# Performance work log

Measured on AMD Instinct MI355X. Metric: run time of the kernel, lower is better.

Reference implementation:

```python
import jax, jax.numpy as jnp
import numpy as np
from jax import lax

DK, K = 3, 3          # duration_kernel_size, kernel_size
PD, P = 1, 1          # duration_padding, padding
RANKS = 3


def setup_inputs() -> dict:
    key = jax.random.key(0)
    k1, k2, k3, k4, k5 = jax.random.split(key, 5)
    B, Cin, Cout, D, H, W = 2, 64, 64, 8, 128, 128
    x = jax.random.normal(k1, (B, Cin, D, H, W), dtype=jnp.float32)
    # 1x1x1 conv weights (squeezed to [out, in])
    head_w = jax.random.normal(k2, (Cout, Cin), dtype=jnp.float32) * 0.1
    tail_w = jax.random.normal(k3, (Cout, Cout), dtype=jnp.float32) * 0.1
    std = float(np.sqrt(2.0 / RANKS))
    U_w = jax.random.normal(k4, (DK * K * K, RANKS), dtype=jnp.float32) * std
    V_w = jax.random.normal(k5, (Cout, RANKS), dtype=jnp.float32) * std
    return {"x": x, "head_w": head_w, "tail_w": tail_w, "U_w": U_w, "V_w": V_w}


def _forward(x, head_w, tail_w, U_w, V_w):
    B, Cin, D, H, W = x.shape
    Cout = head_w.shape[0]
    R = U_w.shape[1]
    # head 1x1x1 conv
    h = jnp.einsum('bidhw,oi->bodhw', x, head_w)
    # replicate pad (torch F.pad mode='replicate' == jnp.pad mode='edge')
    hp = jnp.pad(h, ((0, 0), (0, 0), (PD, PD), (P, P), (P, P)), mode='edge')
    # einsum('bcdhwk,kr->bcdhwr') over unfolded windows == depthwise conv with
    # a kernel shared across channels: fold (B,C) into the batch dim and run a
    # 1->R channel 3D correlation (avoids materializing the [.,27] unfold tensor).
    xin = hp.reshape(B * Cout, 1, D + 2 * PD, H + 2 * P, W + 2 * P)
    kern = U_w.T.reshape(R, 1, DK, K, K)  # unfold flattens as (dk, kh, kw)
    Up = lax.conv_general_dilated(
        xin, kern, window_strides=(1, 1, 1), padding='VALID',
        dimension_numbers=('NCDHW', 'OIDHW', 'NCDHW'))
    Up = Up.reshape(B, Cout, R, D, H, W)
    # _l2norm over rank dim: u / (1e-6 + ||u||_2)
    norm = jnp.sqrt(jnp.sum(Up * Up, axis=2, keepdims=True))
    Un = Up / (1e-6 + norm)
    # V projection: einsum('bcdhwk,cr->brdhwk') with k==1
    Vp = jnp.einsum('bcdhw,cr->brdhw', h, V_w)
    # UV: einsum('bcdhwr,brdhwk->bcdhwk') with k==1 -> contract over r
    UV = jnp.einsum('bcrdhw,brdhw->bcdhw', Un, Vp)
    # tail 1x1x1 conv
    out = jnp.einsum('bcdhw,oc->bodhw', UV, tail_w)
    return out


def reference(x, head_w, tail_w, U_w, V_w):
    return _forward(x, head_w, tail_w, U_w, V_w)
```

## Files before the change

### kernel.cpp

```cpp
#include <hip/hip_runtime.h>

#define Bn   2
#define Cn   64
#define Dd   8
#define Hd   128
#define Wd   128
#define HW   16384
#define DHW  131072
#define NPOS 262144
#define NELEM 16777216

typedef __attribute__((ext_vector_type(8))) short short8;
typedef __attribute__((ext_vector_type(4))) float floatx4;

__device__ __forceinline__ short f2bf(float f) {
    union { float f; unsigned u; } v; v.f = f;
    unsigned r = (v.u + 0x7FFFu + ((v.u >> 16) & 1u)) >> 16;
    return (short)r;
}
__device__ __forceinline__ float bf2f(short s) {
    union { unsigned u; float f; } v; v.u = ((unsigned)(unsigned short)s) << 16;
    return v.f;
}

__global__ __launch_bounds__(256) void k_prep(const float* __restrict__ head_w,
                                              const float* __restrict__ tail_w,
                                              const float* __restrict__ V_w,
                                              short* __restrict__ Whh, short* __restrict__ Whl,
                                              short* __restrict__ Wth, short* __restrict__ Wtl)
{
    int t = threadIdx.x;
#pragma unroll
    for (int rep = 0; rep < 16; ++rep) {
        int idx = rep * 256 + t;
        float wh = head_w[idx];
        short hh = f2bf(wh);
        Whh[idx] = hh; Whl[idx] = f2bf(wh - bf2f(hh));
        float wt = tail_w[idx];
        short th = f2bf(wt);
        Wth[idx] = th; Wtl[idx] = f2bf(wt - bf2f(th));
    }
    if (t < 192) {
        int r = t >> 6, i = t & 63;
        float s = 0.f;
        for (int cc = 0; cc < 64; ++cc) s += V_w[cc * 3 + r] * head_w[cc * 64 + i];
        short hh = f2bf(s);
        Whh[(64 + r) * 64 + i] = hh;
        Whl[(64 + r) * 64 + i] = f2bf(s - bf2f(hh));
    }
#pragma unroll
    for (int rep = 0; rep < 4; ++rep) {
        int idx = rep * 256 + t;
        if (idx < 832) { Whh[67 * 64 + idx] = 0; Whl[67 * 64 + idx] = 0; }
    }
}

__global__ __launch_bounds__(256) void k_headm(const float* __restrict__ x,
                                               const short* __restrict__ Whh,
                                               const short* __restrict__ Whl,
                                               float* __restrict__ h,
                                               float* __restrict__ Vp)
{
    __shared__ short Xh[16 * 64 * 8], Xl[16 * 64 * 8];
    __shared__ short Bh[10 * 64 * 8], Bl[10 * 64 * 8];
    int t  = threadIdx.x;
    int p0 = blockIdx.x * 128;
    int b  = p0 >> 17;
    int s0 = p0 & (DHW - 1);
    const float* xb = x + ((size_t)b * Cn) * DHW + s0;

    int pp = t & 127;
    int ho = t >> 7;
#pragma unroll
    for (int pass = 0; pass < 4; ++pass) {
        int in0 = pass * 16 + ho * 8;
        short8 vh, vl;
#pragma unroll
        for (int j = 0; j < 8; ++j) {
            float f = xb[(size_t)(in0 + j) * DHW + pp];
            short hh = f2bf(f);
            vh[j] = hh; vl[j] = f2bf(f - bf2f(hh));
        }
        int blk  = ((in0 >> 5) << 3) | (pp >> 4);
        int slot = (((in0 >> 3) & 3) << 4) | (pp & 15);
        *(short8*)&Xh[(blk * 64 + slot) * 8] = vh;
        *(short8*)&Xl[(blk * 64 + slot) * 8] = vl;
    }
#pragma unroll
    for (int pass = 0; pass < 3; ++pass) {
        int unit = pass * 256 + t;
        if (unit < 640) {
            int o   = unit - (unit / 80) * 80;
            int oc  = unit / 80;
            int in0 = oc * 8;
            int blk  = ((o >> 4) << 1) | (in0 >> 5);
            int slot = (((in0 >> 3) & 3) << 4) | (o & 15);
            *(short8*)&Bh[(blk * 64 + slot) * 8] = *(const short8*)&Whh[o * 64 + in0];
            *(short8*)&Bl[(blk * 64 + slot) * 8] = *(const short8*)&Whl[o * 64 + in0];
        }
    }
    __syncthreads();

    int lane = t & 63;
    int w    = t >> 6;
    floatx4 acc[2][5];
#pragma unroll
    for (int mt = 0; mt < 2; ++mt)
#pragma unroll
        for (int nt = 0; nt < 5; ++nt) acc[mt][nt] = (floatx4)0.f;

    const short8* XhV = (const short8*)Xh;
    const short8* XlV = (const short8*)Xl;
    const short8* BhV = (const short8*)Bh;
    const short8* BlV = (const short8*)Bl;
#pragma unroll
    for (int ks = 0; ks < 2; ++ks) {
        short8 ah0 = XhV[(ks * 8 + w * 2 + 0) * 64 + lane];
        short8 ah1 = XhV[(ks * 8 + w * 2 + 1) * 64 + lane];
        short8 al0 = XlV[(ks * 8 + w * 2 + 0) * 64 + lane];
        short8 al1 = XlV[(ks * 8 + w * 2 + 1) * 64 + lane];
#pragma unroll
        for (int nt = 0; nt < 5; ++nt) {
            short8 bh = BhV[(nt * 2 + ks) * 64 + lane];
            short8 bl = BlV[(nt * 2 + ks) * 64 + lane];
            acc[0][nt] = __builtin_amdgcn_mfma_f32_16x16x32_bf16(al0, bl, acc[0][nt], 0, 0, 0);
            acc[0][nt] = __builtin_amdgcn_mfma_f32_16x16x32_bf16(al0, bh, acc[0][nt], 0, 0, 0);
            acc[0][nt] = __builtin_amdgcn_mfma_f32_16x16x32_bf16(ah0, bl, acc[0][nt], 0, 0, 0);
            acc[0][nt] = __builtin_amdgcn_mfma_f32_16x16x32_bf16(ah0, bh, acc[0][nt], 0, 0, 0);
            acc[1][nt] = __builtin_amdgcn_mfma_f32_16x16x32_bf16(al1, bl, acc[1][nt], 0, 0, 0);
            acc[1][nt] = __builtin_amdgcn_mfma_f32_16x16x32_bf16(al1, bh, acc[1][nt], 0, 0, 0);
            acc[1][nt] = __builtin_amdgcn_mfma_f32_16x16x32_bf16(ah1, bl, acc[1][nt], 0, 0, 0);
            acc[1][nt] = __builtin_amdgcn_mfma_f32_16x16x32_bf16(ah1, bh, acc[1][nt], 0, 0, 0);
        }
    }

    int outc = lane & 15;
    int quad = lane >> 4;
#pragma unroll
    for (int mt = 0; mt < 2; ++mt) {
#pragma unroll
        for (int nt = 0; nt < 5; ++nt) {
            int o   = nt * 16 + outc;
            int pos = w * 32 + mt * 16 + quad * 4;
            if (o < 64) {
                *(floatx4*)&h[((size_t)(b * Cn + o)) * DHW + s0 + pos] = acc[mt][nt];
            } else if (o < 67) {
                *(floatx4*)&Vp[((size_t)(b * 3 + (o - 64))) * DHW + s0 + pos] = acc[mt][nt];
            }
        }
    }
}

__global__ __launch_bounds__(256) void k_uv(const float* __restrict__ h,
                                            const float* __restrict__ Vp,
                                            const float* __restrict__ U_w,
                                            float* __restrict__ UV)
{
    __shared__ float tile[Dd][4][Wd];

    int blk = blockIdx.x;
    int yt  = blk & 63;
    int bc  = blk >> 6;
    int b   = bc >> 6;
    int y0  = yt * 2;
    int t   = threadIdx.x;

    const float* hb = h + (size_t)bc * DHW;
#pragma unroll
    for (int rep = 0; rep < 4; ++rep) {
        int idx = rep * 256 + t;
        int d   = idx >> 7;
        int rem = idx & 127;
        int yr  = rem >> 5;
        int x4  = (rem & 31) * 4;
        int zy  = y0 - 1 + yr;
        zy = zy < 0 ? 0 : (zy > Hd - 1 ? Hd - 1 : zy);
        *(floatx4*)&tile[d][yr][x4] = *(const floatx4*)(hb + d * HW + zy * Wd + x4);
    }
    __syncthreads();

    int xx = t & 127;
    int yr = t >> 7;
    int y  = y0 + yr;
    int xm = xx - 1; if (xm < 0) xm = 0;
    int xp = xx + 1; if (xp > Wd - 1) xp = Wd - 1;

    const float* vpb = Vp + (size_t)b * 3 * DHW + y * Wd + xx;
    float* uvb       = UV + (size_t)bc * DHW + y * Wd + xx;

    for (int d = 0; d < Dd; ++d) {
        float up0 = 0.f, up1 = 0.f, up2 = 0.f;
#pragma unroll
        for (int dk = 0; dk < 3; ++dk) {
            int zd = d + dk - 1; zd = zd < 0 ? 0 : (zd > Dd - 1 ? Dd - 1 : zd);
#pragma unroll
            for (int kh = 0; kh < 3; ++kh) {
                const float* row = &tile[zd][yr + kh][0];
                float v0 = row[xm], v1 = row[xx], v2 = row[xp];
                int k0 = (dk * 3 + kh) * 3;
                up0 += v0 * U_w[(k0+0)*3 + 0] + v1 * U_w[(k0+1)*3 + 0] + v2 * U_w[(k0+2)*3 + 0];
                up1 += v0 * U_w[(k0+0)*3 + 1] + v1 * U_w[(k0+1)*3 + 1] + v2 * U_w[(k0+2)*3 + 1];
                up2 += v0 * U_w[(k0+0)*3 + 2] + v1 * U_w[(k0+1)*3 + 2] + v2 * U_w[(k0+2)*3 + 2];
            }
        }
        float nrm = sqrtf(up0 * up0 + up1 * up1 + up2 * up2);
        float inv = 1.f / (1e-6f + nrm);
        float uv = (up0 * vpb[(size_t)d * HW]
                  + up1 * vpb[(size_t)DHW + d * HW]
                  + up2 * vpb[(size_t)2 * DHW + d * HW]) * inv;
        uvb[(size_t)d * HW] = uv;
    }
}

__global__ __launch_bounds__(256) void k_tailm(const float* __restrict__ UV,
                                               const short* __restrict__ Wth,
                                               const short* __restrict__ Wtl,
                                               float* __restrict__ out)
{
    __shared__ short Xh[16 * 64 * 8], Xl[16 * 64 * 8];
    __shared__ short Bh[8 * 64 * 8], Bl[8 * 64 * 8];
    int t  = threadIdx.x;
    int p0 = blockIdx.x * 128;
    int b  = p0 >> 17;
    int s0 = p0 & (DHW - 1);
    const float* ub = UV + ((size_t)b * Cn) * DHW + s0;

    int pp = t & 127;
    int ho = t >> 7;
#pragma unroll
    for (int pass = 0; pass < 4; ++pass) {
        int in0 = pass * 16 + ho * 8;
        short8 vh, vl;
#pragma unroll
        for (int j = 0; j < 8; ++j) {
            float f = ub[(size_t)(in0 + j) * DHW + pp];
            short hh = f2bf(f);
            vh[j] = hh; vl[j] = f2bf(f - bf2f(hh));
        }
        int blk  = ((in0 >> 5) << 3) | (pp >> 4);
        int slot = (((in0 >> 3) & 3) << 4) | (pp & 15);
        *(short8*)&Xh[(blk * 64 + slot) * 8] = vh;
        *(short8*)&Xl[(blk * 64 + slot) * 8] = vl;
    }
#pragma unroll
    for (int pass = 0; pass < 2; ++pass) {
        int unit = pass * 256 + t;
        int o    = unit & 63;
        int oc   = unit >> 6;
        int in0  = oc * 8;
        int blk  = ((o >> 4) << 1) | (in0 >> 5);
        int slot = (((in0 >> 3) & 3) << 4) | (o & 15);
        *(short8*)&Bh[(blk * 64 + slot) * 8] = *(const short8*)&Wth[o * 64 + in0];
        *(short8*)&Bl[(blk * 64 + slot) * 8] = *(const short8*)&Wtl[o * 64 + in0];
    }
    __syncthreads();

    int lane = t & 63;
    int w    = t >> 6;
    floatx4 acc[2][4];
#pragma unroll
    for (int mt = 0; mt < 2; ++mt)
#pragma unroll
        for (int nt = 0; nt < 4; ++nt) acc[mt][nt] = (floatx4)0.f;

    const short8* XhV = (const short8*)Xh;
    const short8* XlV = (const short8*)Xl;
    const short8* BhV = (const short8*)Bh;
    const short8* BlV = (const short8*)Bl;
#pragma unroll
    for (int ks = 0; ks < 2; ++ks) {
        short8 ah0 = XhV[(ks * 8 + w * 2 + 0) * 64 + lane];
        short8 ah1 = XhV[(ks * 8 + w * 2 + 1) * 64 + lane];
        short8 al0 = XlV[(ks * 8 + w * 2 + 0) * 64 + lane];
        short8 al1 = XlV[(ks * 8 + w * 2 + 1) * 64 + lane];
#pragma unroll
        for (int nt = 0; nt < 4; ++nt) {
            short8 bh = BhV[(nt * 2 + ks) * 64 + lane];
            short8 bl = BlV[(nt * 2 + ks) * 64 + lane];
            acc[0][nt] = __builtin_amdgcn_mfma_f32_16x16x32_bf16(al0, bl, acc[0][nt], 0, 0, 0);
            acc[0][nt] = __builtin_amdgcn_mfma_f32_16x16x32_bf16(al0, bh, acc[0][nt], 0, 0, 0);
            acc[0][nt] = __builtin_amdgcn_mfma_f32_16x16x32_bf16(ah0, bl, acc[0][nt], 0, 0, 0);
            acc[0][nt] = __builtin_amdgcn_mfma_f32_16x16x32_bf16(ah0, bh, acc[0][nt], 0, 0, 0);
            acc[1][nt] = __builtin_amdgcn_mfma_f32_16x16x32_bf16(al1, bl, acc[1][nt], 0, 0, 0);
            acc[1][nt] = __builtin_amdgcn_mfma_f32_16x16x32_bf16(al1, bh, acc[1][nt], 0, 0, 0);
            acc[1][nt] = __builtin_amdgcn_mfma_f32_16x16x32_bf16(ah1, bl, acc[1][nt], 0, 0, 0);
            acc[1][nt] = __builtin_amdgcn_mfma_f32_16x16x32_bf16(ah1, bh, acc[1][nt], 0, 0, 0);
        }
    }

    int outc = lane & 15;
    int quad = lane >> 4;
#pragma unroll
    for (int mt = 0; mt < 2; ++mt) {
#pragma unroll
        for (int nt = 0; nt < 4; ++nt) {
            int o   = nt * 16 + outc;
            int pos = w * 32 + mt * 16 + quad * 4;
            *(floatx4*)&out[((size_t)(b * Cn + o)) * DHW + s0 + pos] = acc[mt][nt];
        }
    }
}

extern "C" void kernel_launch(void* const* d_in, const int* in_sizes, int n_in,
                              void* d_out, int out_size, void* d_ws, size_t ws_size,
                              hipStream_t stream)
{
    const float* x      = (const float*)d_in[0];
    const float* head_w = (const float*)d_in[1];
    const float* tail_w = (const float*)d_in[2];
    const float* U_w    = (const float*)d_in[3];
    const float* V_w    = (const float*)d_in[4];
    float* out = (float*)d_out;

    float* h   = (float*)d_ws;
    float* Vp  = h + (size_t)NELEM;
    float* UVf = Vp + (size_t)Bn * 3 * DHW;
    short* Whh = (short*)(UVf + (size_t)NELEM);
    short* Whl = Whh + 80 * 64;
    short* Wth = Whl + 80 * 64;
    short* Wtl = Wth + 64 * 64;

    k_prep<<<1, 256, 0, stream>>>(head_w, tail_w, V_w, Whh, Whl, Wth, Wtl);
    k_headm<<<NPOS / 128, 256, 0, stream>>>(x, Whh, Whl, h, Vp);
    k_uv<<<Bn * Cn * (Hd / 2), 256, 0, stream>>>(h, Vp, U_w, UVf);
    k_tailm<<<NPOS / 128, 256, 0, stream>>>(UVf, Wth, Wtl, out);
}
```

Before: 267.2 us.

## Stage GEMM outputs through LDS for coalesced stores; restructure depth conv reuse

The head and tail MFMA kernels now write accumulators into a padded LDS buffer that aliases the input staging area, then store full 128-position rows per channel with coalesced float4 writes. Before, each lane wrote scattered 16-byte fragments. The depthwise U-conv kernel now loads each depth slice's 3x3 neighbourhood once and scatters its contribution into 8 per-depth accumulators, instead of reloading three slices per output depth. The bf16 hi/lo split switches from round-to-nearest to truncation for the high part, which is cheaper, and the low part still carries the residual. The cost is extra LDS traffic, two more barriers, larger shared memory use and more registers in the conv kernel.

```diff
diff --git a/kernel.cpp b/kernel.cpp
--- a/kernel.cpp
+++ b/kernel.cpp
@@ -22,6 +22,14 @@
     union { unsigned u; float f; } v; v.u = ((unsigned)(unsigned short)s) << 16;
     return v.f;
 }
+__device__ __forceinline__ void split2(float f, short& hi, short& lo) {
+    union { float f; unsigned u; } a; a.f = f;
+    unsigned hu = a.u & 0xFFFF0000u;
+    hi = (short)(hu >> 16);
+    union { unsigned u; float f; } hb; hb.u = hu;
+    union { float f; unsigned u; } lb; lb.f = f - hb.f;
+    lo = (short)(lb.u >> 16);
+}
 
 __global__ __launch_bounds__(256) void k_prep(const float* __restrict__ head_w,
                                               const float* __restrict__ tail_w,
@@ -33,20 +41,20 @@
 #pragma unroll
     for (int rep = 0; rep < 16; ++rep) {
         int idx = rep * 256 + t;
-        float wh = head_w[idx];
-        short hh = f2bf(wh);
-        Whh[idx] = hh; Whl[idx] = f2bf(wh - bf2f(hh));
-        float wt = tail_w[idx];
-        short th = f2bf(wt);
-        Wth[idx] = th; Wtl[idx] = f2bf(wt - bf2f(th));
+        short hh, hl;
+        split2(head_w[idx], hh, hl);
+        Whh[idx] = hh; Whl[idx] = hl;
+        split2(tail_w[idx], hh, hl);
+        Wth[idx] = hh; Wtl[idx] = hl;
     }
     if (t < 192) {
         int r = t >> 6, i = t & 63;
         float s = 0.f;
         for (int cc = 0; cc < 64; ++cc) s += V_w[cc * 3 + r] * head_w[cc * 64 + i];
-        short hh = f2bf(s);
+        short hh, hl;
+        split2(s, hh, hl);
         Whh[(64 + r) * 64 + i] = hh;
-        Whl[(64 + r) * 64 + i] = f2bf(s - bf2f(hh));
+        Whl[(64 + r) * 64 + i] = hl;
     }
 #pragma unroll
     for (int rep = 0; rep < 4; ++rep) {
@@ -61,8 +69,13 @@
                                                float* __restrict__ h,
                                                float* __restrict__ Vp)
 {
-    __shared__ short Xh[16 * 64 * 8], Xl[16 * 64 * 8];
-    __shared__ short Bh[10 * 64 * 8], Bl[10 * 64 * 8];
+    __shared__ __align__(16) char smem[52 * 1024];
+    short* Xh = (short*)smem;
+    short* Xl = (short*)(smem + 16 * 1024);
+    short* Bh = (short*)(smem + 32 * 1024);
+    short* Bl = (short*)(smem + 42 * 1024);
+    float* Cb = (float*)smem;
+
     int t  = threadIdx.x;
     int p0 = blockIdx.x * 128;
     int b  = p0 >> 17;
@@ -77,9 +90,9 @@
         short8 vh, vl;
 #pragma unroll
         for (int j = 0; j < 8; ++j) {
-            float f = xb[(size_t)(in0 + j) * DHW + pp];
-            short hh = f2bf(f);
-            vh[j] = hh; vl[j] = f2bf(f - bf2f(hh));
+            short hh, hl;
+            split2(xb[(size_t)(in0 + j) * DHW + pp], hh, hl);
+            vh[j] = hh; vl[j] = hl;
         }
         int blk  = ((in0 >> 5) << 3) | (pp >> 4);
         int slot = (((in0 >> 3) & 3) << 4) | (pp & 15);
@@ -134,19 +147,29 @@
         }
     }
 
+    __syncthreads();
     int outc = lane & 15;
     int quad = lane >> 4;
 #pragma unroll
-    for (int mt = 0; mt < 2; ++mt) {
+    for (int mt = 0; mt < 2; ++mt)
 #pragma unroll
         for (int nt = 0; nt < 5; ++nt) {
             int o   = nt * 16 + outc;
             int pos = w * 32 + mt * 16 + quad * 4;
-            if (o < 64) {
-                *(floatx4*)&h[((size_t)(b * Cn + o)) * DHW + s0 + pos] = acc[mt][nt];
-            } else if (o < 67) {
-                *(floatx4*)&Vp[((size_t)(b * 3 + (o - 64))) * DHW + s0 + pos] = acc[mt][nt];
-            }
+            *(floatx4*)&Cb[o * 132 + pos] = acc[mt][nt];
+        }
+    __syncthreads();
+
+    int xr = (t & 31) * 4;
+    int ob = t >> 5;
+#pragma unroll
+    for (int pass = 0; pass < 9; ++pass) {
+        int o = pass * 8 + ob;
+        floatx4 vv = *(const floatx4*)&Cb[o * 132 + xr];
+        if (o < 64) {
+            *(floatx4*)&h[((size_t)(b * Cn + o)) * DHW + s0 + xr] = vv;
+        } else if (o < 67) {
+            *(floatx4*)&Vp[((size_t)(b * 3 + (o - 64))) * DHW + s0 + xr] = vv;
         }
     }
 }
@@ -185,29 +208,49 @@
     int xm = xx - 1; if (xm < 0) xm = 0;
     int xp = xx + 1; if (xp > Wd - 1) xp = Wd - 1;
 
+    float a0[8], a1[8], a2[8];
+#pragma unroll
+    for (int d = 0; d < 8; ++d) { a0[d] = 0.f; a1[d] = 0.f; a2[d] = 0.f; }
+
+#define CONTRIB(dd, dk)                                                   \
+    {                                                                     \
+        _Pragma("unroll")                                                 \
+        for (int kh = 0; kh < 3; ++kh) {                                  \
+            _Pragma("unroll")                                             \
+            for (int kw = 0; kw < 3; ++kw) {                              \
+                const int kk = (((dk) * 3 + kh) * 3 + kw) * 3;            \
+                a0[dd] += v[kh][kw] * U_w[kk + 0];                        \
+                a1[dd] += v[kh][kw] * U_w[kk + 1];                        \
+                a2[dd] += v[kh][kw] * U_w[kk + 2];                        \
+            }                                                             \
+        }                                                                 \
+    }
+
+#pragma unroll
+    for (int sl = 0; sl < 8; ++sl) {
+        float v[3][3];
+#pragma unroll
+        for (int kh = 0; kh < 3; ++kh) {
+            const float* row = &tile[sl][yr + kh][0];
+            v[kh][0] = row[xm]; v[kh][1] = row[xx]; v[kh][2] = row[xp];
+        }
+        CONTRIB(sl, 1);
+        if (sl == 0) CONTRIB(0, 0);
+        if (sl < 7)  CONTRIB(sl + 1, 0);
+        if (sl > 0)  CONTRIB(sl - 1, 2);
+        if (sl == 7) CONTRIB(7, 2);
+    }
+#undef CONTRIB
+
     const float* vpb = Vp + (size_t)b * 3 * DHW + y * Wd + xx;
     float* uvb       = UV + (size_t)bc * DHW + y * Wd + xx;
-
-    for (int d = 0; d < Dd; ++d) {
-        float up0 = 0.f, up1 = 0.f, up2 = 0.f;
-#pragma unroll
-        for (int dk = 0; dk < 3; ++dk) {
-            int zd = d + dk - 1; zd = zd < 0 ? 0 : (zd > Dd - 1 ? Dd - 1 : zd);
-#pragma unroll
-            for (int kh = 0; kh < 3; ++kh) {
-                const float* row = &tile[zd][yr + kh][0];
-                float v0 = row[xm], v1 = row[xx], v2 = row[xp];
-                int k0 = (dk * 3 + kh) * 3;
-                up0 += v0 * U_w[(k0+0)*3 + 0] + v1 * U_w[(k0+1)*3 + 0] + v2 * U_w[(k0+2)*3 + 0];
-                up1 += v0 * U_w[(k0+0)*3 + 1] + v1 * U_w[(k0+1)*3 + 1] + v2 * U_w[(k0+2)*3 + 1];
-                up2 += v0 * U_w[(k0+0)*3 + 2] + v1 * U_w[(k0+1)*3 + 2] + v2 * U_w[(k0+2)*3 + 2];
-            }
-        }
-        float nrm = sqrtf(up0 * up0 + up1 * up1 + up2 * up2);
+#pragma unroll
+    for (int d = 0; d < 8; ++d) {
+        float nrm = sqrtf(a0[d] * a0[d] + a1[d] * a1[d] + a2[d] * a2[d]);
         float inv = 1.f / (1e-6f + nrm);
-        float uv = (up0 * vpb[(size_t)d * HW]
-                  + up1 * vpb[(size_t)DHW + d * HW]
-                  + up2 * vpb[(size_t)2 * DHW + d * HW]) * inv;
+        float uv = (a0[d] * vpb[(size_t)d * HW]
+                  + a1[d] * vpb[(size_t)DHW + d * HW]
+                  + a2[d] * vpb[(size_t)2 * DHW + d * HW]) * inv;
         uvb[(size_t)d * HW] = uv;
     }
 }
@@ -217,8 +260,13 @@
                                                const short* __restrict__ Wtl,
                                                float* __restrict__ out)
 {
-    __shared__ short Xh[16 * 64 * 8], Xl[16 * 64 * 8];
-    __shared__ short Bh[8 * 64 * 8], Bl[8 * 64 * 8];
+    __shared__ __align__(16) char smem[48 * 1024];
+    short* Xh = (short*)smem;
+    short* Xl = (short*)(smem + 16 * 1024);
+    short* Bh = (short*)(smem + 32 * 1024);
+    short* Bl = (short*)(smem + 40 * 1024);
+    float* Cb = (float*)smem;
+
     int t  = threadIdx.x;
     int p0 = blockIdx.x * 128;
     int b  = p0 >> 17;
@@ -233,9 +281,9 @@
         short8 vh, vl;
 #pragma unroll
         for (int j = 0; j < 8; ++j) {
-            float f = ub[(size_t)(in0 + j) * DHW + pp];
-            short hh = f2bf(f);
-            vh[j] = hh; vl[j] = f2bf(f - bf2f(hh));
+            short hh, hl;
+            split2(ub[(size_t)(in0 + j) * DHW + pp], hh, hl);
+            vh[j] = hh; vl[j] = hl;
         }
         int blk  = ((in0 >> 5) << 3) | (pp >> 4);
         int slot = (((in0 >> 3) & 3) << 4) | (pp & 15);
@@ -288,16 +336,26 @@
         }
     }
 
+    __syncthreads();
     int outc = lane & 15;
     int quad = lane >> 4;
 #pragma unroll
-    for (int mt = 0; mt < 2; ++mt) {
+    for (int mt = 0; mt < 2; ++mt)
 #pragma unroll
         for (int nt = 0; nt < 4; ++nt) {
             int o   = nt * 16 + outc;
             int pos = w * 32 + mt * 16 + quad * 4;
-            *(floatx4*)&out[((size_t)(b * Cn + o)) * DHW + s0 + pos] = acc[mt][nt];
-        }
+            *(floatx4*)&Cb[o * 132 + pos] = acc[mt][nt];
+        }
+    __syncthreads();
+
+    int xr = (t & 31) * 4;
+    int ob = t >> 5;
+#pragma unroll
+    for (int pass = 0; pass < 8; ++pass) {
+        int o = pass * 8 + ob;
+        floatx4 vv = *(const floatx4*)&Cb[o * 132 + xr];
+        *(floatx4*)&out[((size_t)(b * Cn + o)) * DHW + s0 + xr] = vv;
     }
 }
 
```

New measurement: 233.5 us. -12.6%, faster.
